# Performance work log

Hardware: AMD Instinct MI355X
Metric: run time of the kernel (lower is better)

## Reference

```python
import jax, jax.numpy as jnp
import numpy as np

MAX_LEAD = 14
PIL_SEQLEN = 28
TOTAL_LEN = MAX_LEAD + PIL_SEQLEN - 1  # 41
L_MIN = 1.0
L_MAX = 14.0
BANDWIDTH = 0.3
BATCH = 65536


def setup_inputs() -> dict:
    key = jax.random.key(0)
    k1, k2, k3 = jax.random.split(key, 3)
    instock = jax.random.uniform(k1, (BATCH, TOTAL_LEN), dtype=jnp.float32)
    futured_pred = jax.random.uniform(k2, (BATCH, TOTAL_LEN), dtype=jnp.float32)
    lead_pred = jax.random.uniform(k3, (BATCH, 1), dtype=jnp.float32)
    return {"instock": instock, "futured_pred": futured_pred, "lead_pred": lead_pred}


def reference(instock, futured_pred, lead_pred):
    # cumulative sums along time
    futured_cumsum = jnp.cumsum(futured_pred, axis=1)   # [B, T]
    instock_cumsum = jnp.cumsum(instock, axis=1)        # [B, T]

    # running max of (instock_cumsum - futured_cumsum), initialized with relu at t=0.
    # torch loop: o_0 = relu(d_0); o_t = max(d_t, o_{t-1}) == cummax over [relu(d_0), d_1, ...]
    diff = instock_cumsum - futured_cumsum
    head = jnp.maximum(diff[:, :1], 0.0)
    outdate_cumsum = jax.lax.cummax(jnp.concatenate([head, diff[:, 1:]], axis=1), axis=1)  # [B, T]

    # Gaussian-kernel weights over lead-time uncertainty
    lead_scale = lead_pred * (L_MAX - L_MIN) + L_MIN          # L_max != L_min branch
    lead_scale = jnp.clip(lead_scale, L_MIN, L_MAX)[:, :, None]  # [B, 1, 1]
    idx = jnp.arange(1, TOTAL_LEN + 1, dtype=instock.dtype)[None, :, None]   # [1, T, 1]
    kv = jnp.arange(PIL_SEQLEN, dtype=instock.dtype)[None, None, :]          # [1, 1, K]
    z = (idx - (lead_scale + kv)) / BANDWIDTH
    weights_un = jnp.exp(-0.5 * z * z) / BANDWIDTH                            # [B, T, K]
    weights = weights_un / jnp.sum(weights_un, axis=1, keepdims=True)

    # weighted reductions over time dim
    lead_d_cumsum = jnp.einsum('bt,btk->bk', futured_cumsum, weights)
    lead_o_cumsum = jnp.einsum('bt,btk->bk', outdate_cumsum, weights)

    pil = instock_cumsum[:, -1:] - lead_d_cumsum - lead_o_cumsum              # [B, K]
    return pil
```

## Files before the change

kernel.cpp:

```cpp
#include <hip/hip_runtime.h>

#define T_LEN 41
#define K_LEN 28
#define ROWS_PER_BLOCK 8
#define BLOCK 256

#define DPP_ADD(x, ctrl, rmask)                                                  \
    x += __int_as_float(__builtin_amdgcn_update_dpp(                             \
        0, __float_as_int(x), ctrl, rmask, 0xF, false))
#define DPP_MAX(x, ctrl, rmask)                                                  \
    x = fmaxf(x, __int_as_float(__builtin_amdgcn_update_dpp(                     \
        (int)0xFF800000, __float_as_int(x), ctrl, rmask, 0xF, false)))

#define SCAN32_ADD(x)  do { DPP_ADD(x,0x111,0xF); DPP_ADD(x,0x112,0xF);          \
                            DPP_ADD(x,0x114,0xF); DPP_ADD(x,0x118,0xF);          \
                            DPP_ADD(x,0x142,0xA); } while (0)
#define SCAN32_MAX(x)  do { DPP_MAX(x,0x111,0xF); DPP_MAX(x,0x112,0xF);          \
                            DPP_MAX(x,0x114,0xF); DPP_MAX(x,0x118,0xF);          \
                            DPP_MAX(x,0x142,0xA); } while (0)
#define SCAN16_ADD(x)  do { DPP_ADD(x,0x111,0xF); DPP_ADD(x,0x112,0xF);          \
                            DPP_ADD(x,0x114,0xF); DPP_ADD(x,0x118,0xF); } while (0)
#define SCAN16_MAX(x)  do { DPP_MAX(x,0x111,0xF); DPP_MAX(x,0x112,0xF);          \
                            DPP_MAX(x,0x114,0xF); DPP_MAX(x,0x118,0xF); } while (0)

#define BCAST32(x, sel) __int_as_float(                                          \
    __builtin_amdgcn_ds_swizzle(__float_as_int(x), ((sel) << 5)))

__global__ __launch_bounds__(BLOCK) void pil_kernel(
    const float* __restrict__ instock,
    const float* __restrict__ futured,
    const float* __restrict__ lead_pred,
    float* __restrict__ out, int B)
{
    __shared__ float2 lds[ROWS_PER_BLOCK][T_LEN];

    const int g    = threadIdx.x >> 5;
    const int lane = threadIdx.x & 31;
    const int row  = blockIdx.x * ROWS_PER_BLOCK + g;

    const float lead = lead_pred[row];

    const float* __restrict__ f = futured + row * T_LEN;
    const float* __restrict__ s = instock + row * T_LEN;

    float fa = f[lane];
    float sa = s[lane];
    float fb = 0.f, sb = 0.f;
    if (lane < T_LEN - 32) { fb = f[32 + lane]; sb = s[32 + lane]; }

    SCAN32_ADD(fa);
    SCAN32_ADD(sa);
    const float fc31 = BCAST32(fa, 31);
    const float ic31 = BCAST32(sa, 31);
    SCAN16_ADD(fb);
    SCAN16_ADD(sb);
    fb += fc31;
    sb += ic31;
    const float ic41 = BCAST32(sb, 8);

    float da = sa - fa;
    if (lane == 0) da = fmaxf(da, 0.f);
    SCAN32_MAX(da);
    const float m31 = BCAST32(da, 31);
    float db = sb - fb;
    SCAN16_MAX(db);
    db = fmaxf(db, m31);

    lds[g][lane] = make_float2(fa, da);
    if (lane < T_LEN - 32) lds[g][32 + lane] = make_float2(fb, db);

    __syncthreads();

    if (lane < K_LEN) {
        const float ls = fminf(fmaxf(lead * 13.0f + 1.0f, 1.0f), 14.0f);
        const float Ff = floorf(ls);
        const float r  = ls - Ff;
        const int   Fi = (int)Ff;
        const float inv_bw = 1.0f / 0.3f;

        float wsum = 0.f, accd = 0.f, acco = 0.f;
        #pragma unroll
        for (int j = -1; j <= 2; ++j) {
            const int i = Fi + lane + j;
            const float dz = ((float)j - r) * inv_bw;
            const float w  = __expf(-0.5f * dz * dz);
            if (i >= 1 && i <= T_LEN) {
                const float2 p = lds[g][i - 1];
                wsum += w;
                accd = fmaf(w, p.x, accd);
                acco = fmaf(w, p.y, acco);
            }
        }
        out[row * K_LEN + lane] = ic41 - (accd + acco) / wsum;
    }
}

extern "C" void kernel_launch(void* const* d_in, const int* in_sizes, int n_in,
                              void* d_out, int out_size, void* d_ws, size_t ws_size,
                              hipStream_t stream) {
    const float* instock   = (const float*)d_in[0];
    const float* futured   = (const float*)d_in[1];
    const float* lead_pred = (const float*)d_in[2];
    float* out = (float*)d_out;
    (void)d_ws; (void)ws_size;

    const int B = in_sizes[0] / T_LEN;
    const int grid = B / ROWS_PER_BLOCK;

    pil_kernel<<<grid, BLOCK, 0, stream>>>(instock, futured, lead_pred, out, B);
}
```

Baseline: 76.51 us.

## Process two rows per half-wave and fuse cumsum-plus-cummax into one LDS value

Each 32-lane group now handles two rows, and the scans for both rows are interleaved so their DPP chains can overlap. It scans the difference instock minus futured directly, derives the final instock total from the two sums, and stores only futured_cumsum plus outdate_cumsum in a zero-padded LDS row. Padding removes the bounds branch on the loads, and the __syncthreads is dropped because each group only reads its own data. The cost is more registers per thread and half as many blocks, which may reduce latency hiding.

```diff
diff --git a/kernel.cpp b/kernel.cpp
--- a/kernel.cpp
+++ b/kernel.cpp
@@ -2,8 +2,11 @@
 
 #define T_LEN 41
 #define K_LEN 28
-#define ROWS_PER_BLOCK 8
+#define GROUPS 8
+#define RPG 2
+#define ROWS_PER_BLOCK (GROUPS * RPG)
 #define BLOCK 256
+#define P_STRIDE 45
 
 #define DPP_ADD(x, ctrl, rmask)                                                  \
     x += __int_as_float(__builtin_amdgcn_update_dpp(                             \
@@ -32,66 +35,87 @@
     const float* __restrict__ lead_pred,
     float* __restrict__ out, int B)
 {
-    __shared__ float2 lds[ROWS_PER_BLOCK][T_LEN];
+    __shared__ float lds[GROUPS][RPG][P_STRIDE];
 
     const int g    = threadIdx.x >> 5;
     const int lane = threadIdx.x & 31;
-    const int row  = blockIdx.x * ROWS_PER_BLOCK + g;
+    const int row0 = blockIdx.x * ROWS_PER_BLOCK + g * RPG;
 
-    const float lead = lead_pred[row];
+    float fa[RPG], ga[RPG], fb[RPG], gb[RPG], lead[RPG];
 
-    const float* __restrict__ f = futured + row * T_LEN;
-    const float* __restrict__ s = instock + row * T_LEN;
+    #pragma unroll
+    for (int r = 0; r < RPG; ++r) {
+        const float* __restrict__ f = futured + (row0 + r) * T_LEN;
+        const float* __restrict__ s = instock + (row0 + r) * T_LEN;
+        const float fv = f[lane];
+        const float sv = s[lane];
+        float fbv = 0.f, sbv = 0.f;
+        if (lane < T_LEN - 32) { fbv = f[32 + lane]; sbv = s[32 + lane]; }
+        lead[r] = lead_pred[row0 + r];
+        fa[r] = fv; ga[r] = sv - fv;
+        fb[r] = fbv; gb[r] = sbv - fbv;
+    }
 
-    float fa = f[lane];
-    float sa = s[lane];
-    float fb = 0.f, sb = 0.f;
-    if (lane < T_LEN - 32) { fb = f[32 + lane]; sb = s[32 + lane]; }
+    #pragma unroll
+    for (int r = 0; r < RPG; ++r) SCAN32_ADD(fa[r]);
+    #pragma unroll
+    for (int r = 0; r < RPG; ++r) SCAN32_ADD(ga[r]);
 
-    SCAN32_ADD(fa);
-    SCAN32_ADD(sa);
-    const float fc31 = BCAST32(fa, 31);
-    const float ic31 = BCAST32(sa, 31);
-    SCAN16_ADD(fb);
-    SCAN16_ADD(sb);
-    fb += fc31;
-    sb += ic31;
-    const float ic41 = BCAST32(sb, 8);
+    float ic41[RPG];
+    #pragma unroll
+    for (int r = 0; r < RPG; ++r) {
+        const float fc31 = BCAST32(fa[r], 31);
+        const float gc31 = BCAST32(ga[r], 31);
+        SCAN16_ADD(fb[r]);
+        SCAN16_ADD(gb[r]);
+        fb[r] += fc31;
+        gb[r] += gc31;
+        ic41[r] = BCAST32(fb[r] + gb[r], 8);
+    }
 
-    float da = sa - fa;
-    if (lane == 0) da = fmaxf(da, 0.f);
-    SCAN32_MAX(da);
-    const float m31 = BCAST32(da, 31);
-    float db = sb - fb;
-    SCAN16_MAX(db);
-    db = fmaxf(db, m31);
+    #pragma unroll
+    for (int r = 0; r < RPG; ++r) {
+        if (lane == 0) ga[r] = fmaxf(ga[r], 0.f);
+        SCAN32_MAX(ga[r]);
+    }
+    #pragma unroll
+    for (int r = 0; r < RPG; ++r) {
+        const float m31 = BCAST32(ga[r], 31);
+        SCAN16_MAX(gb[r]);
+        gb[r] = fmaxf(gb[r], m31);
+    }
 
-    lds[g][lane] = make_float2(fa, da);
-    if (lane < T_LEN - 32) lds[g][32 + lane] = make_float2(fb, db);
-
-    __syncthreads();
+    #pragma unroll
+    for (int r = 0; r < RPG; ++r) {
+        lds[g][r][2 + lane] = fa[r] + ga[r];
+        if (lane < T_LEN - 32) {
+            lds[g][r][34 + lane] = fb[r] + gb[r];
+        } else if (lane < 13) {
+            const int slot = (lane < 11) ? (lane - 9) : (lane + 32);
+            lds[g][r][slot] = 0.f;
+        }
+    }
 
     if (lane < K_LEN) {
-        const float ls = fminf(fmaxf(lead * 13.0f + 1.0f, 1.0f), 14.0f);
-        const float Ff = floorf(ls);
-        const float r  = ls - Ff;
-        const int   Fi = (int)Ff;
-        const float inv_bw = 1.0f / 0.3f;
+        #pragma unroll
+        for (int r = 0; r < RPG; ++r) {
+            const float ls = fminf(fmaxf(lead[r] * 13.0f + 1.0f, 1.0f), 14.0f);
+            const float Ff = floorf(ls);
+            const float fr = ls - Ff;
+            const int   Fi = (int)Ff;
+            const float inv_bw = 1.0f / 0.3f;
 
-        float wsum = 0.f, accd = 0.f, acco = 0.f;
-        #pragma unroll
-        for (int j = -1; j <= 2; ++j) {
-            const int i = Fi + lane + j;
-            const float dz = ((float)j - r) * inv_bw;
-            const float w  = __expf(-0.5f * dz * dz);
-            if (i >= 1 && i <= T_LEN) {
-                const float2 p = lds[g][i - 1];
-                wsum += w;
-                accd = fmaf(w, p.x, accd);
-                acco = fmaf(w, p.y, acco);
+            float wsum = 0.f, acc = 0.f;
+            #pragma unroll
+            for (int j = -1; j <= 2; ++j) {
+                const int   i  = Fi + lane + j;
+                const float dz = ((float)j - fr) * inv_bw;
+                const float w  = __expf(-0.5f * dz * dz);
+                acc = fmaf(w, lds[g][r][i + 1], acc);
+                if (i >= 1 && i <= T_LEN) wsum += w;
             }
+            out[(row0 + r) * K_LEN + lane] = ic41[r] - acc / wsum;
         }
-        out[row * K_LEN + lane] = ic41 - (accd + acco) / wsum;
     }
 }
 
@@ -102,7 +126,7 @@
     const float* futured   = (const float*)d_in[1];
     const float* lead_pred = (const float*)d_in[2];
     float* out = (float*)d_out;
-    (void)d_ws; (void)ws_size;
+    (void)d_ws; (void)ws_size; (void)n_in; (void)out_size;
 
     const int B = in_sizes[0] / T_LEN;
     const int grid = B / ROWS_PER_BLOCK;
```

Measured after the change: 78.03 us. About the same (+2.0%).
